# Kernel optimization log

Hardware: AMD Instinct MI355X
Metric: run time of the kernel (lower is better)

Reference implementation:

```python
import jax, jax.numpy as jnp
import numpy as np

I_, J_, D_IN, D_H = 100, 8, 768, 64
N_NODES, N_HE, N_INC, N_CELLS, VOCAB = 160000, 320000, 1600000, 800, 30000
BN_EPS = 1e-5


def setup_inputs() -> dict:
    key = jax.random.key(0)
    ks = jax.random.split(key, 20)
    w = lambda k, s: jax.random.normal(k, s, jnp.float32) * 0.05
    inp = {}
    inp['x'] = jax.random.normal(ks[0], (I_, J_, D_IN), jnp.float32)
    inp['node_tokens'] = jax.random.randint(ks[1], (N_NODES,), 0, VOCAB)
    inp['inc_node'] = jax.random.randint(ks[2], (N_INC,), 0, N_NODES)
    inp['inc_hedge'] = jnp.sort(jax.random.randint(ks[3], (N_INC,), 0, N_HE))
    inp['node2cell'] = jnp.sort(jax.random.randint(ks[4], (N_NODES,), 0, N_CELLS))
    inp['vac_emb'] = w(ks[5], (VOCAB, D_IN))
    inp['fhi_w'] = w(ks[6], (D_IN, D_H)); inp['fhi_b'] = jnp.zeros((D_H,), jnp.float32)
    inp['fin_w'] = w(ks[7], (D_IN, D_H)); inp['fin_b'] = jnp.zeros((D_H,), jnp.float32)
    inp['th1'] = w(ks[8], (D_H, D_H)); inp['b1'] = jnp.zeros((D_H,), jnp.float32)
    inp['th2'] = w(ks[9], (D_H, D_H)); inp['b2'] = jnp.zeros((D_H,), jnp.float32)
    for li, k in zip((1, 2, 3), (ks[10], ks[11], ks[12])):
        inp[f'wc{li}'] = w(k, (D_H, D_H, 3))
        inp[f'bc{li}'] = jnp.zeros((D_H,), jnp.float32)
        inp[f'g{li}'] = jnp.ones((D_H,), jnp.float32)
        inp[f'be{li}'] = jnp.zeros((D_H,), jnp.float32)
        inp[f'm{li}'] = jnp.zeros((D_H,), jnp.float32)
        inp[f'v{li}'] = jnp.ones((D_H,), jnp.float32)
    inp['fct_w'] = w(ks[13], (D_H, D_H)); inp['fct_b'] = jnp.zeros((D_H,), jnp.float32)
    return inp


def _inv_safe(c):
    return jnp.where(c > 0, 1.0 / jnp.maximum(c, 1.0), 0.0)


def _hconv(xf, inc_node, inc_hedge, theta, bias):
    # PyG HypergraphConv (no attention): D^{-1} H W B^{-1} H^T (X Theta) + bias
    xt = xf @ theta                                        # [N, D]
    ones = jnp.ones((inc_node.shape[0],), xt.dtype)
    deg_e = jax.ops.segment_sum(ones, inc_hedge, N_HE)     # B_e
    he = jax.ops.segment_sum(xt[inc_node], inc_hedge, N_HE) * _inv_safe(deg_e)[:, None]
    deg_v = jax.ops.segment_sum(ones, inc_node, N_NODES)   # D_v
    out = jax.ops.segment_sum(he[inc_hedge], inc_node, N_NODES) * _inv_safe(deg_v)[:, None]
    return out + bias


def _conv_bn(h, wc, bc, g, be, m, v):
    # Conv1d(k=3, pad=1) -> ReLU -> BatchNorm1d (inference stats); dropout is eval-mode identity
    h = jax.lax.conv_general_dilated(h, wc, (1,), [(1, 1)],
                                     dimension_numbers=('NCH', 'OIH', 'NCH')) + bc[None, :, None]
    h = jax.nn.relu(h)
    return (h - m[None, :, None]) * (g[None, :, None] / jnp.sqrt(v[None, :, None] + BN_EPS)) + be[None, :, None]


def _forward(x, node_tokens, inc_node, inc_hedge, node2cell, vac_emb, fhi_w, fhi_b,
             fin_w, fin_b, th1, b1, th2, b2, wc1, bc1, g1, be1, m1, v1,
             wc2, bc2, g2, be2, m2, v2, wc3, bc3, g3, be3, m3, v3, fct_w, fct_b):
    # x = fin(x)
    x0 = jnp.einsum('ijd,dh->ijh', x, fin_w) + fin_b       # [100, 8, 64]
    # node_features = fhi(graph_embedding[graph.x])  (gather-dominated)
    nf = vac_emb[node_tokens] @ fhi_w + fhi_b              # [N, 64]
    # two HypergraphConv layers with residuals (eval-mode dropout = identity)
    h1 = jax.nn.relu(_hconv(nf, inc_node, inc_hedge, th1, b1)) + nf
    gx = jax.nn.relu(_hconv(h1, inc_node, inc_hedge, th2, b2)) + nf
    # per-graph mean + max pooling (graph.batch is all-zero per graph => one vector per cell)
    cnt = jax.ops.segment_sum(jnp.ones((N_NODES,), gx.dtype), node2cell, N_CELLS)
    mean_p = jax.ops.segment_sum(gx, node2cell, N_CELLS) * _inv_safe(cnt)[:, None]
    max_p = jax.ops.segment_max(gx, node2cell, N_CELLS)
    max_p = jnp.where(cnt[:, None] > 0, max_p, 0.0)
    cell_emb = 0.5 * (mean_p + max_p)                      # [800, 64]
    x_upd = x0 + 0.3 * cell_emb.reshape(I_, J_, D_H)       # x[i,j] += 0.3*graph_emb
    h = jnp.transpose(x_upd, (0, 2, 1))                    # [100, 64, 8]
    h = _conv_bn(h, wc1, bc1, g1, be1, m1, v1)
    h = _conv_bn(h, wc2, bc2, g2, be2, m2, v2)
    h = _conv_bn(h, wc3, bc3, g3, be3, m3, v3)
    out2 = jnp.mean(h, axis=2) @ fct_w + fct_b             # [100, 64]
    return x_upd, out2


def reference(x, node_tokens, inc_node, inc_hedge, node2cell, vac_emb, fhi_w, fhi_b,
              fin_w, fin_b, th1, b1, th2, b2, wc1, bc1, g1, be1, m1, v1,
              wc2, bc2, g2, be2, m2, v2, wc3, bc3, g3, be3, m3, v3, fct_w, fct_b):
    return _forward(x, node_tokens, inc_node, inc_hedge, node2cell, vac_emb, fhi_w, fhi_b,
                    fin_w, fin_b, th1, b1, th2, b2, wc1, bc1, g1, be1, m1, v1,
                    wc2, bc2, g2, be2, m2, v2, wc3, bc3, g3, be3, m3, v3, fct_w, fct_b)
```

## Files before the change

### kernel.cpp

```cpp
#include <hip/hip_runtime.h>
#include <hip/hip_bf16.h>
#include <cstdint>
#include <cstddef>

#define I_      100
#define J_      8
#define D_IN    768
#define D_H     64
#define N_NODES 160000
#define N_HE    320000
#define N_INC   1600000
#define N_CELLS 800
#define VOCAB   30000

#define NRANGE   256
#define NPR      625
#define EPB      (N_INC / 256)

typedef unsigned short u16;
using short8 = __attribute__((ext_vector_type(8))) short;
using f32x4  = __attribute__((ext_vector_type(4))) float;

__device__ __forceinline__ float bf2f(u16 u) {
    union { uint32_t i; float f; } x; x.i = ((uint32_t)u) << 16; return x.f;
}
__device__ __forceinline__ u16 f2bf(float f) {
    union { float f; uint32_t i; } x; x.f = f;
    uint32_t b = x.i;
    b += 0x7FFFu + ((b >> 16) & 1u);
    return (u16)(b >> 16);
}
__device__ __forceinline__ float lo_bf(uint32_t u) {
    union { uint32_t i; float f; } x; x.i = u << 16; return x.f;
}
__device__ __forceinline__ float hi_bf(uint32_t u) {
    union { uint32_t i; float f; } x; x.i = u & 0xFFFF0000u; return x.f;
}
__device__ __forceinline__ uint32_t pack_bf2(float a, float b) {
    return (uint32_t)f2bf(a) | ((uint32_t)f2bf(b) << 16);
}

#define G_OFF_HE   (N_INC / 256)
#define G_OFF_CELL (N_NODES / 256)
#define G_CONV_BIG ((D_IN * 64) / 256)
#define G_CONV_SM  ((64 * 64) / 256)
#define G_KA       256
#define G_KC       256
#define G_KD       256
#define G_PGEMM    ((VOCAB + 63) / 64)
#define G_XT       (N_NODES / 64)
#define G_X0       ((I_ * J_ + 63) / 64)
#define G_HEDGE    (N_HE / 32)
#define G_NODE     (N_NODES / 32)

__device__ __forceinline__ void dev_offsets(int bid, const int* __restrict__ sorted,
                                            int n, int nbins, int* __restrict__ off) {
    int i = bid * 256 + threadIdx.x;
    if (i >= n) return;
    int cur = sorted[i];
    int prev = (i == 0) ? -1 : sorted[i - 1];
    for (int b = prev + 1; b <= cur; ++b) off[b] = i;
    if (i == n - 1) {
        for (int b = cur + 1; b <= nbins; ++b) off[b] = n;
    }
}

__device__ __forceinline__ void dev_convT(int bid, const float* __restrict__ B,
                                          u16* __restrict__ Bt, int K) {
    int g = bid * 256 + threadIdx.x;
    if (g >= K * 64) return;
    int k = g >> 6, n = g & 63;
    Bt[(size_t)n * K + k] = f2bf(B[g]);
}

__device__ __forceinline__ void dev_ka(int bid, const int* __restrict__ inc_node,
                                       int* __restrict__ counts, int* __restrict__ lds) {
    int tid = threadIdx.x;
    lds[tid] = 0;
    __syncthreads();
    int s = bid * EPB, e = s + EPB;
    for (int i = s + tid; i < e; i += 256)
        atomicAdd(&lds[(unsigned)inc_node[i] / NPR], 1);
    __syncthreads();
    counts[bid * NRANGE + tid] = lds[tid];
}

__device__ __forceinline__ void dev_kb(const int* __restrict__ counts,
                                       int* __restrict__ chunk_off,
                                       int* __restrict__ range_base,
                                       int* __restrict__ lds) {
    int r = threadIdx.x;
    int run = 0;
    for (int b = 0; b < 256; ++b) {
        chunk_off[b * NRANGE + r] = run;
        run += counts[b * NRANGE + r];
    }
    lds[r] = run;
    __syncthreads();
    int s = run;
    #pragma unroll
    for (int d = 1; d < 256; d <<= 1) {
        int t = (r >= d) ? lds[r - d] : 0;
        __syncthreads();
        lds[r] += t;
        __syncthreads();
    }
    int base = lds[r] - s;
    range_base[r] = base;
    if (r == 255) range_base[256] = lds[255];
    for (int b = 0; b < 256; ++b) chunk_off[b * NRANGE + r] += base;
}

__device__ __forceinline__ void dev_kc(int bid, const int* __restrict__ inc_node,
                                       const int* __restrict__ inc_hedge,
                                       const int* __restrict__ chunk_off,
                                       int2* __restrict__ bucket, int* __restrict__ lds) {
    int tid = threadIdx.x;
    lds[tid] = 0;
    __syncthreads();
    int s = bid * EPB, e = s + EPB;
    const int* co = chunk_off + bid * NRANGE;
    for (int i = s + tid; i < e; i += 256) {
        int v = inc_node[i];
        int h = inc_hedge[i];
        int rg = (unsigned)v / NPR;
        int rank = atomicAdd(&lds[rg], 1);
        bucket[co[rg] + rank] = make_int2(v, h);
    }
}

__device__ __forceinline__ void dev_kd(int r, const int2* __restrict__ bucket,
                                       const int* __restrict__ range_base,
                                       int* __restrict__ node_off, int* __restrict__ csr,
                                       int* __restrict__ lds) {
    int tid = threadIdx.x;
    int* hist = lds;
    int* tsum = lds + 768;
    int* cur  = lds + 1024;
    for (int i = tid; i < 768; i += 256) { hist[i] = 0; cur[i] = 0; }
    __syncthreads();
    int lo = r * NPR;
    int pb = range_base[r], pe = range_base[r + 1];
    for (int i = pb + tid; i < pe; i += 256)
        atomicAdd(&hist[bucket[i].x - lo], 1);
    __syncthreads();
    int b3 = tid * 3;
    int a0 = hist[b3], a1 = hist[b3 + 1], a2 = hist[b3 + 2];
    int s = a0 + a1 + a2;
    tsum[tid] = s;
    __syncthreads();
    #pragma unroll
    for (int d = 1; d < 256; d <<= 1) {
        int t = (tid >= d) ? tsum[tid - d] : 0;
        __syncthreads();
        tsum[tid] += t;
        __syncthreads();
    }
    int excl = tsum[tid] - s;
    hist[b3]     = excl;
    hist[b3 + 1] = excl + a0;
    hist[b3 + 2] = excl + a0 + a1;
    __syncthreads();
    for (int v = tid; v < NPR; v += 256) node_off[lo + v] = pb + hist[v];
    if (r == NRANGE - 1 && tid == 0) node_off[N_NODES] = N_INC;
    for (int i = pb + tid; i < pe; i += 256) {
        int2 p = bucket[i];
        int l = p.x - lo;
        int k = atomicAdd(&cur[l], 1);
        csr[pb + hist[l] + k] = p.y;
    }
}

template <int BF16_OUT, int GATHER, int KK>
__device__ __forceinline__ void dev_gemm_direct(int wid, const float* __restrict__ A,
                                                const int* __restrict__ tok,
                                                const u16* __restrict__ Bt,
                                                const float* __restrict__ bias,
                                                void* __restrict__ C, int M) {
    int lane = threadIdx.x & 63;
    int m16 = lane & 15, q = lane >> 4;
    int base = wid << 4;
    if (base >= M) return;
    int row = base + m16;
    const float* arow = GATHER ? (A + ((size_t)tok[row] << 6))
                               : (A + (size_t)row * KK);

    f32x4 acc0 = {0.f, 0.f, 0.f, 0.f};
    f32x4 acc1 = {0.f, 0.f, 0.f, 0.f};
    f32x4 acc2 = {0.f, 0.f, 0.f, 0.f};
    f32x4 acc3 = {0.f, 0.f, 0.f, 0.f};

    #pragma unroll 2
    for (int kt = 0; kt < KK; kt += 32) {
        const float* ap = arow + kt + q * 8;
        float4 av0 = *reinterpret_cast<const float4*>(ap);
        float4 av1 = *reinterpret_cast<const float4*>(ap + 4);
        short8 a;
        a[0] = (short)f2bf(av0.x); a[1] = (short)f2bf(av0.y);
        a[2] = (short)f2bf(av0.z); a[3] = (short)f2bf(av0.w);
        a[4] = (short)f2bf(av1.x); a[5] = (short)f2bf(av1.y);
        a[6] = (short)f2bf(av1.z); a[7] = (short)f2bf(av1.w);
        const u16* bp = Bt + (size_t)m16 * KK + kt + q * 8;
        short8 b0 = *reinterpret_cast<const short8*>(bp);
        short8 b1 = *reinterpret_cast<const short8*>(bp + (size_t)16 * KK);
        short8 b2 = *reinterpret_cast<const short8*>(bp + (size_t)32 * KK);
        short8 b3 = *reinterpret_cast<const short8*>(bp + (size_t)48 * KK);
        acc0 = __builtin_amdgcn_mfma_f32_16x16x32_bf16(a, b0, acc0, 0, 0, 0);
        acc1 = __builtin_amdgcn_mfma_f32_16x16x32_bf16(a, b1, acc1, 0, 0, 0);
        acc2 = __builtin_amdgcn_mfma_f32_16x16x32_bf16(a, b2, acc2, 0, 0, 0);
        acc3 = __builtin_amdgcn_mfma_f32_16x16x32_bf16(a, b3, acc3, 0, 0, 0);
    }

    f32x4 accs[4] = {acc0, acc1, acc2, acc3};
    #pragma unroll
    for (int r = 0; r < 4; ++r) {
        int gr = base + q * 4 + r;
        #pragma unroll
        for (int j = 0; j < 4; ++j) {
            int col = j * 16 + m16;
            float v = accs[j][r];
            if (!BF16_OUT) v += bias[col];
            if (BF16_OUT)
                ((u16*)C)[(size_t)gr * 64 + col] = f2bf(v);
            else
                ((float*)C)[(size_t)gr * 64 + col] = v;
        }
    }
}

__device__ __forceinline__ void dev_hedge_sum(int bid, const int* __restrict__ inc_node,
                                              const int* __restrict__ he_off,
                                              const u16* __restrict__ xt,
                                              u16* __restrict__ he) {
    int w = (bid * 256 + (int)threadIdx.x) >> 6;
    int lane = threadIdx.x & 63;
    int sub = lane >> 3;
    int c8 = (lane & 7) << 3;
    int hedge = w * 8 + sub;
    if (hedge >= N_HE) return;
    int s = he_off[hedge], e = he_off[hedge + 1];

    float a0 = 0.f, a1 = 0.f, a2 = 0.f, a3 = 0.f;
    float a4 = 0.f, a5 = 0.f, a6 = 0.f, a7 = 0.f;

    int idx = (s < e) ? inc_node[s] : 0;
    for (int j = s; j < e; ++j) {
        int cur = idx;
        if (j + 1 < e) idx = inc_node[j + 1];
        uint4 d = *reinterpret_cast<const uint4*>(xt + (((size_t)cur) << 6) + c8);
        a0 += lo_bf(d.x); a1 += hi_bf(d.x);
        a2 += lo_bf(d.y); a3 += hi_bf(d.y);
        a4 += lo_bf(d.z); a5 += hi_bf(d.z);
        a6 += lo_bf(d.w); a7 += hi_bf(d.w);
    }

    float inv = (e > s) ? 1.f / (float)(e - s) : 0.f;
    uint4 o;
    o.x = pack_bf2(a0 * inv, a1 * inv);
    o.y = pack_bf2(a2 * inv, a3 * inv);
    o.z = pack_bf2(a4 * inv, a5 * inv);
    o.w = pack_bf2(a6 * inv, a7 * inv);
    *reinterpret_cast<uint4*>(he + (((size_t)hedge) << 6) + c8) = o;
}

__device__ __forceinline__ void dev_node_sum(int bid, const int* __restrict__ csr,
                                             const int* __restrict__ node_off,
                                             const u16* __restrict__ he,
                                             const float* __restrict__ bias,
                                             const float* __restrict__ P,
                                             const int* __restrict__ tok,
                                             float* __restrict__ out) {
    int w = (bid * 256 + (int)threadIdx.x) >> 6;
    int lane = threadIdx.x & 63;
    int sub = lane >> 3;
    int c8 = (lane & 7) << 3;
    int node = w * 8 + sub;
    if (node >= N_NODES) return;
    int s = node_off[node], e = node_off[node + 1];

    float a0 = 0.f, a1 = 0.f, a2 = 0.f, a3 = 0.f;
    float a4 = 0.f, a5 = 0.f, a6 = 0.f, a7 = 0.f;

    int idx = (s < e) ? csr[s] : 0;
    for (int j = s; j < e; ++j) {
        int cur = idx;
        if (j + 1 < e) idx = csr[j + 1];
        uint4 d = *reinterpret_cast<const uint4*>(he + (((size_t)cur) << 6) + c8);
        a0 += lo_bf(d.x); a1 += hi_bf(d.x);
        a2 += lo_bf(d.y); a3 += hi_bf(d.y);
        a4 += lo_bf(d.z); a5 += hi_bf(d.z);
        a6 += lo_bf(d.w); a7 += hi_bf(d.w);
    }

    float inv = (e > s) ? 1.f / (float)(e - s) : 0.f;
    const float* nfp = P + (((size_t)tok[node]) << 6) + c8;
    float4 nv0 = *reinterpret_cast<const float4*>(nfp);
    float4 nv1 = *reinterpret_cast<const float4*>(nfp + 4);
    float4 o0, o1;
    o0.x = fmaxf(fmaf(a0, inv, bias[c8 + 0]), 0.f) + nv0.x;
    o0.y = fmaxf(fmaf(a1, inv, bias[c8 + 1]), 0.f) + nv0.y;
    o0.z = fmaxf(fmaf(a2, inv, bias[c8 + 2]), 0.f) + nv0.z;
    o0.w = fmaxf(fmaf(a3, inv, bias[c8 + 3]), 0.f) + nv0.w;
    o1.x = fmaxf(fmaf(a4, inv, bias[c8 + 4]), 0.f) + nv1.x;
    o1.y = fmaxf(fmaf(a5, inv, bias[c8 + 5]), 0.f) + nv1.y;
    o1.z = fmaxf(fmaf(a6, inv, bias[c8 + 6]), 0.f) + nv1.z;
    o1.w = fmaxf(fmaf(a7, inv, bias[c8 + 7]), 0.f) + nv1.w;
    float* op = out + (((size_t)node) << 6) + c8;
    *reinterpret_cast<float4*>(op) = o0;
    *reinterpret_cast<float4*>(op + 4) = o1;
}

__global__ __launch_bounds__(256) void k_p1(const int* __restrict__ inc_hedge,
                                            const int* __restrict__ node2cell,
                                            const int* __restrict__ inc_node,
                                            int* __restrict__ he_off, int* __restrict__ cell_off,
                                            int* __restrict__ counts,
                                            const float* __restrict__ fhi_w, const float* __restrict__ fin_w,
                                            const float* __restrict__ th1, const float* __restrict__ th2,
                                            u16* __restrict__ Bt_fhi, u16* __restrict__ Bt_fin,
                                            u16* __restrict__ Bt_th1, u16* __restrict__ Bt_th2) {
    __shared__ int lds[256];
    int bid = blockIdx.x;
    if (bid < G_OFF_HE) { dev_offsets(bid, inc_hedge, N_INC, N_HE, he_off); return; }
    bid -= G_OFF_HE;
    if (bid < G_KA) { dev_ka(bid, inc_node, counts, lds); return; }
    bid -= G_KA;
    if (bid < G_OFF_CELL) { dev_offsets(bid, node2cell, N_NODES, N_CELLS, cell_off); return; }
    bid -= G_OFF_CELL;
    if (bid < G_CONV_BIG) { dev_convT(bid, fhi_w, Bt_fhi, D_IN); return; }
    bid -= G_CONV_BIG;
    if (bid < G_CONV_BIG) { dev_convT(bid, fin_w, Bt_fin, D_IN); return; }
    bid -= G_CONV_BIG;
    if (bid < G_CONV_SM) { dev_convT(bid, th1, Bt_th1, 64); return; }
    bid -= G_CONV_SM;
    dev_convT(bid, th2, Bt_th2, 64);
}

__global__ __launch_bounds__(256) void k_p2(const int* __restrict__ counts,
                                            int* __restrict__ chunk_off, int* __restrict__ range_base,
                                            const float* __restrict__ vac_emb,
                                            const u16* __restrict__ Bt_fhi,
                                            const float* __restrict__ fhi_b, float* __restrict__ P) {
    __shared__ int lds[256];
    int bid = blockIdx.x;
    if (bid < G_PGEMM) {
        int wid = bid * 4 + ((int)threadIdx.x >> 6);
        dev_gemm_direct<0, 0, D_IN>(wid, vac_emb, nullptr, Bt_fhi, fhi_b, P, VOCAB);
        return;
    }
    dev_kb(counts, chunk_off, range_base, lds);
}

__global__ __launch_bounds__(256) void k_p3(const float* __restrict__ P,
                                            const int* __restrict__ tok,
                                            const u16* __restrict__ Bt_th1, u16* __restrict__ xt,
                                            const int* __restrict__ inc_node,
                                            const int* __restrict__ inc_hedge,
                                            const int* __restrict__ chunk_off,
                                            int2* __restrict__ bucket,
                                            const float* __restrict__ x, const u16* __restrict__ Bt_fin,
                                            const float* __restrict__ fin_b, float* __restrict__ x0) {
    __shared__ int lds[256];
    int bid = blockIdx.x;
    if (bid < G_XT) {
        int wid = bid * 4 + ((int)threadIdx.x >> 6);
        dev_gemm_direct<1, 1, 64>(wid, P, tok, Bt_th1, nullptr, xt, N_NODES);
        return;
    }
    bid -= G_XT;
    if (bid < G_KC) { dev_kc(bid, inc_node, inc_hedge, chunk_off, bucket, lds); return; }
    bid -= G_KC;
    {
        int wid = bid * 4 + ((int)threadIdx.x >> 6);
        dev_gemm_direct<0, 0, D_IN>(wid, x, nullptr, Bt_fin, fin_b, x0, I_ * J_);
    }
}

__global__ __launch_bounds__(256) void k_p4(const int* __restrict__ inc_node,
                                            const int* __restrict__ he_off,
                                            const u16* __restrict__ xt, u16* __restrict__ he,
                                            const int2* __restrict__ bucket,
                                            const int* __restrict__ range_base,
                                            int* __restrict__ node_off, int* __restrict__ csr) {
    __shared__ int lds[1792];
    int bid = blockIdx.x;
    if (bid < G_HEDGE) { dev_hedge_sum(bid, inc_node, he_off, xt, he); return; }
    bid -= G_HEDGE;
    dev_kd(bid, bucket, range_base, node_off, csr, lds);
}

__global__ __launch_bounds__(256) void k_xt2(const float* __restrict__ A,
                                             const u16* __restrict__ Bt,
                                             u16* __restrict__ xt) {
    int wid = blockIdx.x * 4 + ((int)threadIdx.x >> 6);
    dev_gemm_direct<1, 0, 64>(wid, A, nullptr, Bt, nullptr, xt, N_NODES);
}

__global__ __launch_bounds__(256) void k_hedge_sum(const int* __restrict__ inc_node,
                                                   const int* __restrict__ he_off,
                                                   const u16* __restrict__ xt,
                                                   u16* __restrict__ he) {
    dev_hedge_sum(blockIdx.x, inc_node, he_off, xt, he);
}

__global__ __launch_bounds__(256) void k_node_sum(const int* __restrict__ csr,
                                                  const int* __restrict__ node_off,
                                                  const u16* __restrict__ he,
                                                  const float* __restrict__ bias,
                                                  const float* __restrict__ P,
                                                  const int* __restrict__ tok,
                                                  float* __restrict__ out) {
    dev_node_sum(blockIdx.x, csr, node_off, he, bias, P, tok, out);
}

__global__ __launch_bounds__(256) void k_pool(const float* __restrict__ gx,
                                              const int* __restrict__ cell_off,
                                              const float* __restrict__ x0,
                                              float* __restrict__ out1) {
    __shared__ float ssum[4][64];
    __shared__ float smax[4][64];
    int c = blockIdx.x;
    int lane = threadIdx.x & 63;
    int w = threadIdx.x >> 6;
    int s = cell_off[c], e = cell_off[c + 1];
    float sum = 0.f, mx = -INFINITY;
    for (int n = s + w; n < e; n += 4) {
        float v = gx[((size_t)n << 6) + lane];
        sum += v;
        mx = fmaxf(mx, v);
    }
    ssum[w][lane] = sum;
    smax[w][lane] = mx;
    __syncthreads();
    if (w == 0) {
        sum = ssum[0][lane] + ssum[1][lane] + ssum[2][lane] + ssum[3][lane];
        mx = fmaxf(fmaxf(smax[0][lane], smax[1][lane]), fmaxf(smax[2][lane], smax[3][lane]));
        int cnt = e - s;
        float mean = (cnt > 0) ? sum / (float)cnt : 0.f;
        float mp = (cnt > 0) ? mx : 0.f;
        float ce = 0.5f * (mean + mp);
        out1[((size_t)c << 6) + lane] = x0[((size_t)c << 6) + lane] + 0.3f * ce;
    }
}

__global__ __launch_bounds__(256) void k_tcn(
    const float* __restrict__ xu,
    const float* __restrict__ wc1, const float* __restrict__ bc1, const float* __restrict__ g1,
    const float* __restrict__ be1, const float* __restrict__ m1, const float* __restrict__ v1,
    const float* __restrict__ wc2, const float* __restrict__ bc2, const float* __restrict__ g2,
    const float* __restrict__ be2, const float* __restrict__ m2, const float* __restrict__ v2,
    const float* __restrict__ wc3, const float* __restrict__ bc3, const float* __restrict__ g3,
    const float* __restrict__ be3, const float* __restrict__ m3, const float* __restrict__ v3,
    const float* __restrict__ fct_w, const float* __restrict__ fct_b,
    float* __restrict__ out2) {
    __shared__ float w_lds[64 * 64 * 3];
    __shared__ float hA[64][10];
    __shared__ float hB[64][10];
    __shared__ float mo[64];

    int n = blockIdx.x, tid = threadIdx.x;

    if (tid < 64) {
        hA[tid][0] = 0.f; hA[tid][9] = 0.f;
        hB[tid][0] = 0.f; hB[tid][9] = 0.f;
    }
    #pragma unroll
    for (int l = tid; l < 512; l += 256) {
        int t = l >> 6, i = l & 63;
        hA[i][t + 1] = xu[(size_t)n * 512 + l];
    }

    const float* wcs[3] = {wc1, wc2, wc3};
    const float* bcs[3] = {bc1, bc2, bc3};
    const float* gs[3]  = {g1, g2, g3};
    const float* bes[3] = {be1, be2, be3};
    const float* ms[3]  = {m1, m2, m3};
    const float* vs[3]  = {v1, v2, v3};

    float (*hin)[10] = hA;
    float (*hout)[10] = hB;

    #pragma unroll
    for (int li = 0; li < 3; ++li) {
        for (int l = tid; l < 64 * 64 * 3; l += 256) w_lds[l] = wcs[li][l];
        __syncthreads();
        #pragma unroll
        for (int rep = 0; rep < 2; ++rep) {
            int idx = tid + rep * 256;
            int o = idx >> 3, t = idx & 7;
            float acc = bcs[li][o];
            #pragma unroll 8
            for (int i = 0; i < 64; ++i) {
                const float* wr = &w_lds[o * 192 + i * 3];
                acc = fmaf(hin[i][t + 0], wr[0], acc);
                acc = fmaf(hin[i][t + 1], wr[1], acc);
                acc = fmaf(hin[i][t + 2], wr[2], acc);
            }
            acc = fmaxf(acc, 0.f);
            float sc = gs[li][o] * rsqrtf(vs[li][o] + 1e-5f);
            acc = (acc - ms[li][o]) * sc + bes[li][o];
            hout[o][t + 1] = acc;
        }
        __syncthreads();
        float (*tmp)[10] = hin; hin = hout; hout = tmp;
    }

    if (tid < 64) {
        float s = 0.f;
        #pragma unroll
        for (int t = 0; t < 8; ++t) s += hin[tid][t + 1];
        mo[tid] = s * 0.125f;
    }
    __syncthreads();
    if (tid < 64) {
        float acc = fct_b[tid];
        #pragma unroll 8
        for (int o = 0; o < 64; ++o) acc = fmaf(mo[o], fct_w[o * 64 + tid], acc);
        out2[(size_t)n * 64 + tid] = acc;
    }
}

extern "C" void kernel_launch(void* const* d_in, const int* in_sizes, int n_in,
                              void* d_out, int out_size, void* d_ws, size_t ws_size,
                              hipStream_t stream) {
    (void)in_sizes; (void)n_in; (void)out_size; (void)ws_size;

    const float* x          = (const float*)d_in[0];
    const int*   node_tok   = (const int*)d_in[1];
    const int*   inc_node   = (const int*)d_in[2];
    const int*   inc_hedge  = (const int*)d_in[3];
    const int*   node2cell  = (const int*)d_in[4];
    const float* vac_emb    = (const float*)d_in[5];
    const float* fhi_w      = (const float*)d_in[6];
    const float* fhi_b      = (const float*)d_in[7];
    const float* fin_w      = (const float*)d_in[8];
    const float* fin_b      = (const float*)d_in[9];
    const float* th1        = (const float*)d_in[10];
    const float* b1         = (const float*)d_in[11];
    const float* th2        = (const float*)d_in[12];
    const float* b2         = (const float*)d_in[13];
    const float* fct_w      = (const float*)d_in[32];
    const float* fct_b      = (const float*)d_in[33];

    char* ws = (char*)d_ws;
    size_t off = 0;
    float* P        = (float*)(ws + off); off += (size_t)VOCAB * 64 * 4;
    float* hbuf     = (float*)(ws + off); off += (size_t)N_NODES * 64 * 4;
    u16*   xt       = (u16*)(ws + off);   off += (size_t)N_NODES * 64 * 2;
    u16*   he       = (u16*)(ws + off);   off += (size_t)N_HE * 64 * 2;
    int2*  bucket   = (int2*)(ws + off);  off += (size_t)N_INC * 8;
    float* x0       = (float*)(ws + off); off += (size_t)N_CELLS * 64 * 4;
    u16*   Bt_fhi   = (u16*)(ws + off);   off += (size_t)64 * D_IN * 2;
    u16*   Bt_fin   = (u16*)(ws + off);   off += (size_t)64 * D_IN * 2;
    u16*   Bt_th1   = (u16*)(ws + off);   off += (size_t)64 * 64 * 2;
    u16*   Bt_th2   = (u16*)(ws + off);   off += (size_t)64 * 64 * 2;
    int*   he_off   = (int*)(ws + off);   off += ((size_t)(N_HE + 1) * 4 + 255) / 256 * 256;
    int*   node_off = (int*)(ws + off);   off += ((size_t)(N_NODES + 1) * 4 + 255) / 256 * 256;
    int*   csr      = (int*)(ws + off);   off += (size_t)N_INC * 4;
    int*   cell_off = (int*)(ws + off);   off += ((size_t)(N_CELLS + 1) * 4 + 255) / 256 * 256;

    int*  counts     = (int*)hbuf;
    int*  chunk_off  = counts + 256 * 256;
    int*  range_base = chunk_off + 256 * 256;

    float* out1 = (float*)d_out;
    float* out2 = out1 + (size_t)I_ * J_ * D_H;

    k_p1<<<G_OFF_HE + G_KA + G_OFF_CELL + 2 * G_CONV_BIG + 2 * G_CONV_SM, 256, 0, stream>>>(
        inc_hedge, node2cell, inc_node, he_off, cell_off, counts,
        fhi_w, fin_w, th1, th2, Bt_fhi, Bt_fin, Bt_th1, Bt_th2);

    k_p2<<<G_PGEMM + 1, 256, 0, stream>>>(counts, chunk_off, range_base,
                                          vac_emb, Bt_fhi, fhi_b, P);

    k_p3<<<G_XT + G_KC + G_X0, 256, 0, stream>>>(P, node_tok, Bt_th1, xt,
                                                 inc_node, inc_hedge, chunk_off, bucket,
                                                 x, Bt_fin, fin_b, x0);

    k_p4<<<G_HEDGE + G_KD, 256, 0, stream>>>(inc_node, he_off, xt, he,
                                             bucket, range_base, node_off, csr);

    k_node_sum<<<G_NODE, 256, 0, stream>>>(csr, node_off, he, b1, P, node_tok, hbuf);

    k_xt2<<<G_XT, 256, 0, stream>>>(hbuf, Bt_th2, xt);

    k_hedge_sum<<<G_HEDGE, 256, 0, stream>>>(inc_node, he_off, xt, he);

    k_node_sum<<<G_NODE, 256, 0, stream>>>(csr, node_off, he, b2, P, node_tok, hbuf);

    k_pool<<<N_CELLS, 256, 0, stream>>>(hbuf, cell_off, x0, out1);

    k_tcn<<<I_, 256, 0, stream>>>(out1,
        (const float*)d_in[14], (const float*)d_in[15], (const float*)d_in[16],
        (const float*)d_in[17], (const float*)d_in[18], (const float*)d_in[19],
        (const float*)d_in[20], (const float*)d_in[21], (const float*)d_in[22],
        (const float*)d_in[23], (const float*)d_in[24], (const float*)d_in[25],
        (const float*)d_in[26], (const float*)d_in[27], (const float*)d_in[28],
        (const float*)d_in[29], (const float*)d_in[30], (const float*)d_in[31],
        fct_w, fct_b, out2);
}
```

Baseline: 544.8 us.

## Split GEMM output columns across waves and move x0 GEMM into p2

```diff
diff --git a/kernel.cpp b/kernel.cpp
--- a/kernel.cpp
+++ b/kernel.cpp
@@ -47,9 +47,9 @@
 #define G_KA       256
 #define G_KC       256
 #define G_KD       256
-#define G_PGEMM    ((VOCAB + 63) / 64)
-#define G_XT       (N_NODES / 64)
-#define G_X0       ((I_ * J_ + 63) / 64)
+#define G_PGEMM    (VOCAB / 16)
+#define G_XT       (N_NODES / 16)
+#define G_X0       ((I_ * J_) / 16)
 #define G_HEDGE    (N_HE / 32)
 #define G_NODE     (N_NODES / 32)
 
@@ -172,59 +172,53 @@
 }
 
 template <int BF16_OUT, int GATHER, int KK>
-__device__ __forceinline__ void dev_gemm_direct(int wid, const float* __restrict__ A,
-                                                const int* __restrict__ tok,
-                                                const u16* __restrict__ Bt,
-                                                const float* __restrict__ bias,
-                                                void* __restrict__ C, int M) {
+__device__ __forceinline__ void dev_gemm_cs(int wid, const float* __restrict__ A,
+                                            const int* __restrict__ tok,
+                                            const u16* __restrict__ Bt,
+                                            const float* __restrict__ bias,
+                                            void* __restrict__ C, int M) {
     int lane = threadIdx.x & 63;
     int m16 = lane & 15, q = lane >> 4;
-    int base = wid << 4;
+    int rg = wid >> 2, jb = wid & 3;
+    int base = rg << 4;
     if (base >= M) return;
     int row = base + m16;
     const float* arow = GATHER ? (A + ((size_t)tok[row] << 6))
                                : (A + (size_t)row * KK);
-
-    f32x4 acc0 = {0.f, 0.f, 0.f, 0.f};
-    f32x4 acc1 = {0.f, 0.f, 0.f, 0.f};
-    f32x4 acc2 = {0.f, 0.f, 0.f, 0.f};
-    f32x4 acc3 = {0.f, 0.f, 0.f, 0.f};
-
-    #pragma unroll 2
+    const u16* brow = Bt + (size_t)(jb * 16 + m16) * KK + q * 8;
+    const float* ap = arow + q * 8;
+
+    f32x4 acc = {0.f, 0.f, 0.f, 0.f};
+    float4 a0 = *reinterpret_cast<const float4*>(ap);
+    float4 a1 = *reinterpret_cast<const float4*>(ap + 4);
+
+    #pragma unroll 4
     for (int kt = 0; kt < KK; kt += 32) {
-        const float* ap = arow + kt + q * 8;
-        float4 av0 = *reinterpret_cast<const float4*>(ap);
-        float4 av1 = *reinterpret_cast<const float4*>(ap + 4);
+        float4 n0, n1;
+        if (kt + 32 < KK) {
+            n0 = *reinterpret_cast<const float4*>(ap + kt + 32);
+            n1 = *reinterpret_cast<const float4*>(ap + kt + 36);
+        }
         short8 a;
-        a[0] = (short)f2bf(av0.x); a[1] = (short)f2bf(av0.y);
-        a[2] = (short)f2bf(av0.z); a[3] = (short)f2bf(av0.w);
-        a[4] = (short)f2bf(av1.x); a[5] = (short)f2bf(av1.y);
-        a[6] = (short)f2bf(av1.z); a[7] = (short)f2bf(av1.w);
-        const u16* bp = Bt + (size_t)m16 * KK + kt + q * 8;
-        short8 b0 = *reinterpret_cast<const short8*>(bp);
-        short8 b1 = *reinterpret_cast<const short8*>(bp + (size_t)16 * KK);
-        short8 b2 = *reinterpret_cast<const short8*>(bp + (size_t)32 * KK);
-        short8 b3 = *reinterpret_cast<const short8*>(bp + (size_t)48 * KK);
-        acc0 = __builtin_amdgcn_mfma_f32_16x16x32_bf16(a, b0, acc0, 0, 0, 0);
-        acc1 = __builtin_amdgcn_mfma_f32_16x16x32_bf16(a, b1, acc1, 0, 0, 0);
-        acc2 = __builtin_amdgcn_mfma_f32_16x16x32_bf16(a, b2, acc2, 0, 0, 0);
-        acc3 = __builtin_amdgcn_mfma_f32_16x16x32_bf16(a, b3, acc3, 0, 0, 0);
-    }
-
-    f32x4 accs[4] = {acc0, acc1, acc2, acc3};
+        a[0] = (short)f2bf(a0.x); a[1] = (short)f2bf(a0.y);
+        a[2] = (short)f2bf(a0.z); a[3] = (short)f2bf(a0.w);
+        a[4] = (short)f2bf(a1.x); a[5] = (short)f2bf(a1.y);
+        a[6] = (short)f2bf(a1.z); a[7] = (short)f2bf(a1.w);
+        short8 b = *reinterpret_cast<const short8*>(brow + kt);
+        acc = __builtin_amdgcn_mfma_f32_16x16x32_bf16(a, b, acc, 0, 0, 0);
+        a0 = n0; a1 = n1;
+    }
+
     #pragma unroll
     for (int r = 0; r < 4; ++r) {
         int gr = base + q * 4 + r;
-        #pragma unroll
-        for (int j = 0; j < 4; ++j) {
-            int col = j * 16 + m16;
-            float v = accs[j][r];
-            if (!BF16_OUT) v += bias[col];
-            if (BF16_OUT)
-                ((u16*)C)[(size_t)gr * 64 + col] = f2bf(v);
-            else
-                ((float*)C)[(size_t)gr * 64 + col] = v;
-        }
+        int col = jb * 16 + m16;
+        float v = acc[r];
+        if (!BF16_OUT) v += bias[col];
+        if (BF16_OUT)
+            ((u16*)C)[(size_t)gr * 64 + col] = f2bf(v);
+        else
+            ((float*)C)[(size_t)gr * 64 + col] = v;
     }
 }
 
@@ -340,12 +334,20 @@
                                             int* __restrict__ chunk_off, int* __restrict__ range_base,
                                             const float* __restrict__ vac_emb,
                                             const u16* __restrict__ Bt_fhi,
-                                            const float* __restrict__ fhi_b, float* __restrict__ P) {
+                                            const float* __restrict__ fhi_b, float* __restrict__ P,
+                                            const float* __restrict__ x, const u16* __restrict__ Bt_fin,
+                                            const float* __restrict__ fin_b, float* __restrict__ x0) {
     __shared__ int lds[256];
     int bid = blockIdx.x;
     if (bid < G_PGEMM) {
         int wid = bid * 4 + ((int)threadIdx.x >> 6);
-        dev_gemm_direct<0, 0, D_IN>(wid, vac_emb, nullptr, Bt_fhi, fhi_b, P, VOCAB);
+        dev_gemm_cs<0, 0, D_IN>(wid, vac_emb, nullptr, Bt_fhi, fhi_b, P, VOCAB);
+        return;
+    }
+    bid -= G_PGEMM;
+    if (bid < G_X0) {
+        int wid = bid * 4 + ((int)threadIdx.x >> 6);
+        dev_gemm_cs<0, 0, D_IN>(wid, x, nullptr, Bt_fin, fin_b, x0, I_ * J_);
         return;
     }
     dev_kb(counts, chunk_off, range_base, lds);
@@ -357,23 +359,16 @@
                                             const int* __restrict__ inc_node,
                                             const int* __restrict__ inc_hedge,
                                             const int* __restrict__ chunk_off,
-                                            int2* __restrict__ bucket,
-                                            const float* __restrict__ x, const u16* __restrict__ Bt_fin,
-                                            const float* __restrict__ fin_b, float* __restrict__ x0) {
+                                            int2* __restrict__ bucket) {
     __shared__ int lds[256];
     int bid = blockIdx.x;
     if (bid < G_XT) {
         int wid = bid * 4 + ((int)threadIdx.x >> 6);
-        dev_gemm_direct<1, 1, 64>(wid, P, tok, Bt_th1, nullptr, xt, N_NODES);
+        dev_gemm_cs<1, 1, 64>(wid, P, tok, Bt_th1, nullptr, xt, N_NODES);
         return;
     }
     bid -= G_XT;
-    if (bid < G_KC) { dev_kc(bid, inc_node, inc_hedge, chunk_off, bucket, lds); return; }
-    bid -= G_KC;
-    {
-        int wid = bid * 4 + ((int)threadIdx.x >> 6);
-        dev_gemm_direct<0, 0, D_IN>(wid, x, nullptr, Bt_fin, fin_b, x0, I_ * J_);
-    }
+    dev_kc(bid, inc_node, inc_hedge, chunk_off, bucket, lds);
 }
 
 __global__ __launch_bounds__(256) void k_p4(const int* __restrict__ inc_node,
@@ -393,7 +388,7 @@
                                              const u16* __restrict__ Bt,
                                              u16* __restrict__ xt) {
     int wid = blockIdx.x * 4 + ((int)threadIdx.x >> 6);
-    dev_gemm_direct<1, 0, 64>(wid, A, nullptr, Bt, nullptr, xt, N_NODES);
+    dev_gemm_cs<1, 0, 64>(wid, A, nullptr, Bt, nullptr, xt, N_NODES);
 }
 
 __global__ __launch_bounds__(256) void k_hedge_sum(const int* __restrict__ inc_node,
@@ -570,12 +565,12 @@
         inc_hedge, node2cell, inc_node, he_off, cell_off, counts,
         fhi_w, fin_w, th1, th2, Bt_fhi, Bt_fin, Bt_th1, Bt_th2);
 
-    k_p2<<<G_PGEMM + 1, 256, 0, stream>>>(counts, chunk_off, range_base,
-                                          vac_emb, Bt_fhi, fhi_b, P);
-
-    k_p3<<<G_XT + G_KC + G_X0, 256, 0, stream>>>(P, node_tok, Bt_th1, xt,
-                                                 inc_node, inc_hedge, chunk_off, bucket,
+    k_p2<<<G_PGEMM + G_X0 + 1, 256, 0, stream>>>(counts, chunk_off, range_base,
+                                                 vac_emb, Bt_fhi, fhi_b, P,
                                                  x, Bt_fin, fin_b, x0);
+
+    k_p3<<<G_XT + G_KC, 256, 0, stream>>>(P, node_tok, Bt_th1, xt,
+                                          inc_node, inc_hedge, chunk_off, bucket);
 
     k_p4<<<G_HEDGE + G_KD, 256, 0, stream>>>(inc_node, he_off, xt, he,
                                              bucket, range_base, node_off, csr);
```

Measured after the change: 616.9 us. +13.2%, slower.
